# Optimization experiments

Measured on AMD Instinct MI355X. Metric: run time of the kernel, lower is better.

## Reference

```python
import jax, jax.numpy as jnp
import numpy as np

BITS = 256      # bits per token
HEADS = 8       # num voting heads
NPOS = 4        # n_position_bits for RELATIVE encoder (binary code of distance)
MAXD = 8        # max_distance of position encoder
NBPN = 12       # n_bits_per_neuron = min(similarity_bits, 12)
SEQ = 2048      # number of tokens
SIM = 2 * BITS + NPOS  # similarity_bits


def setup_inputs() -> dict:
    key = jax.random.key(0)
    k1, k2, k3 = jax.random.split(key, 3)
    tokens = jax.random.randint(k1, (SEQ, BITS), 0, 2, dtype=jnp.int32)
    head_idx = jax.random.randint(k2, (HEADS, NBPN), 0, SIM, dtype=jnp.int32)
    # RAM table contents: one bit (0/1) per address per head (trained lookup table)
    table = jax.random.bernoulli(k3, 0.5, (HEADS, 2 ** NBPN)).astype(jnp.float32)
    return {"tokens": tokens, "head_idx": head_idx, "table": table}


def reference(tokens, head_idx, table):
    S, B = tokens.shape
    H, K = head_idx.shape
    w = (2 ** jnp.arange(K)).astype(jnp.int32)  # slot weight 2^k per selected bit

    # relative-distance binary code table for distances 0..MAXD  -> (MAXD+1, NPOS)
    d_vals = jnp.arange(MAXD + 1)
    rel_bits = ((d_vals[:, None] >> jnp.arange(NPOS)[None, :]) & 1).astype(jnp.int32)

    # which source each selected bit position comes from within cat([query,key,rel])
    mask_q = (head_idx < B)
    mask_k = (head_idx >= B) & (head_idx < 2 * B)
    mask_r = head_idx >= 2 * B

    qg = tokens[:, jnp.clip(head_idx, 0, B - 1)]            # (S, H, K)
    kg = tokens[:, jnp.clip(head_idx - B, 0, B - 1)]        # (S, H, K)
    rg = rel_bits[:, jnp.clip(head_idx - 2 * B, 0, NPOS - 1)]  # (MAXD+1, H, K)

    # separable address contributions (query / key / relative distance)
    Aq = jnp.einsum('shk,hk->sh', qg, (mask_q * w).astype(jnp.int32))  # (S, H)
    Ak = jnp.einsum('shk,hk->sh', kg, (mask_k * w).astype(jnp.int32))  # (S, H)
    Ar = jnp.einsum('dhk,hk->dh', rg, (mask_r * w).astype(jnp.int32))  # (MAXD+1, H)

    i = jnp.arange(S)
    dist = jnp.clip(i[:, None] - i[None, :], 0, MAXD)        # (S, S)
    addr = Aq[:, None, :] + Ak[None, :, :] + Ar[dist]        # (S, S, H)

    head_votes = table[jnp.arange(H)[None, None, :], addr]   # (S, S, H)
    tril = (i[None, :] <= i[:, None]).astype(table.dtype)    # j > i gets vote 0
    votes = head_votes.sum(-1) * tril                        # (S, S)

    thr = H // 2
    attended = (votes >= thr).astype(table.dtype)            # (S, S)
    included = attended.sum(-1)                              # (S,)

    tok_f = tokens.astype(table.dtype)
    # XOR of selected tokens == per-bit parity of their sum
    parity = jnp.mod(attended @ tok_f, 2.0)                  # (S, B)
    # fallback: first token with max vote when nothing crossed the threshold
    fallback = tok_f[jnp.argmax(votes, axis=-1)]             # (S, B)
    return jnp.where((included > 0)[:, None], parity, fallback)
```

## Files before the change

kernel.cpp:

```cpp
#include <hip/hip_runtime.h>
#include <stdint.h>

#define SEQ   2048
#define BITS  256
#define HEADS 8
#define NPOS  4
#define MAXD  8
#define NBPN  12

typedef unsigned long long u64;
typedef unsigned int       u32;
typedef unsigned short     u16;

#define OFF_TBL    0
#define OFF_PACKED 4096
#define OFF_AQ     (4096 + 65536)
#define OFF_AK     (4096 + 65536 + 32768)
#define OFF_AR     (4096 + 65536 + 65536)

__global__ __launch_bounds__(256) void prep_kernel(
        const int* __restrict__ tokens, const int* __restrict__ head_idx,
        const float* __restrict__ table,
        u64* __restrict__ tblbits, u64* __restrict__ packed,
        u16* __restrict__ Aq, u16* __restrict__ Ak, u16* __restrict__ Ar) {
    const int bid = blockIdx.x, tid = threadIdx.x;
    if (bid < 2048) {
        int t = bid * 256 + tid;
        u64 m = __ballot(tokens[t] & 1);
        if ((tid & 63) == 0) packed[t >> 6] = m;
    } else if (bid < 2048 + 128) {
        int t = (bid - 2048) * 256 + tid;
        u64 m = __ballot(table[t] != 0.0f);
        if ((tid & 63) == 0) tblbits[t >> 6] = m;
    } else {
        int t = (bid - 2176) * 256 + tid;
        int s = t >> 3, h = t & 7;
        const int* hi  = head_idx + h * NBPN;
        const int* tok = tokens + s * BITS;
        int aq = 0, ak = 0;
        #pragma unroll
        for (int k = 0; k < NBPN; ++k) {
            int idx = hi[k];
            if (idx < BITS)          aq += tok[idx] << k;
            else if (idx < 2 * BITS) ak += tok[idx - BITS] << k;
        }
        Aq[t] = (u16)aq;
        Ak[t] = (u16)ak;
        if (t < (MAXD + 1) * HEADS) {
            int d = t / HEADS, hh = t % HEADS;
            const int* hi2 = head_idx + hh * NBPN;
            int ar = 0;
            #pragma unroll
            for (int k = 0; k < NBPN; ++k) {
                int idx = hi2[k];
                if (idx >= 2 * BITS) ar += ((d >> (idx - 2 * BITS)) & 1) << k;
            }
            Ar[t] = (u16)ar;
        }
    }
}

__device__ inline u64 shfl_down_u64(u64 x, int o) {
    u32 lo = (u32)x, hi = (u32)(x >> 32);
    lo = __shfl_down(lo, o, 64);
    hi = __shfl_down(hi, o, 64);
    return ((u64)hi << 32) | lo;
}

__global__ __launch_bounds__(128) void row_kernel(
        const u64* __restrict__ tblbits, const u64* __restrict__ packed,
        const u16* __restrict__ Aq, const u16* __restrict__ Ak,
        const u16* __restrict__ Ar, float* __restrict__ out) {

    __shared__ u32 tbl[HEADS * 128];
    __shared__ u16 aqar[MAXD + 1][HEADS];
    __shared__ u64 p_acc[2][4];
    __shared__ int p_inc[2];
    __shared__ u64 p_key[2];

    const int i   = blockIdx.x;
    const int tid = threadIdx.x;

    const u32* tb32 = (const u32*)tblbits;
    #pragma unroll
    for (int w = 0; w < 8; ++w) tbl[tid + w * 128] = tb32[tid + w * 128];
    if (tid < (MAXD + 1) * HEADS) {
        int h = tid & 7;
        aqar[tid >> 3][h] = (u16)(Aq[i * HEADS + h] + Ar[tid]);
    }
    __syncthreads();

    u32 a8[8];
    #pragma unroll
    for (int h = 0; h < 8; ++h) a8[h] = aqar[MAXD][h];

    u64 acc0 = 0, acc1 = 0, acc2 = 0, acc3 = 0;
    int inc = 0;
    u64 bestkey = 0;

    for (int j = tid; j <= i; j += 128) {
        int dist = i - j;
        const uint4 akv = *(const uint4*)(Ak + j * HEADS);
        int votes = 0;
        if (__any(dist < MAXD)) {
            #pragma unroll
            for (int h = 0; h < 8; ++h) {
                u32 ak_h = ((&akv.x)[h >> 1] >> ((h & 1) * 16)) & 0xFFFFu;
                u32 base = (dist >= MAXD) ? a8[h] : (u32)aqar[dist][h];
                u32 addr = base + ak_h;
                votes += (int)((tbl[(h << 7) + (addr >> 5)] >> (addr & 31)) & 1u);
            }
        } else {
            #pragma unroll
            for (int h = 0; h < 8; ++h) {
                u32 ak_h = ((&akv.x)[h >> 1] >> ((h & 1) * 16)) & 0xFFFFu;
                u32 addr = a8[h] + ak_h;
                votes += (int)((tbl[(h << 7) + (addr >> 5)] >> (addr & 31)) & 1u);
            }
        }
        int att = (votes >= HEADS / 2) ? 1 : 0;
        u64 m = (u64)0 - (u64)att;
        const ulonglong2* pj = (const ulonglong2*)(packed + j * 4);
        ulonglong2 pA = pj[0], pB = pj[1];
        acc0 ^= pA.x & m; acc1 ^= pA.y & m;
        acc2 ^= pB.x & m; acc3 ^= pB.y & m;
        inc += att;
        u64 key = ((u64)(votes + 1) << 32) | (u64)(0x7FFFFFFF - j);
        if (key > bestkey) bestkey = key;
    }

    #pragma unroll
    for (int o = 32; o > 0; o >>= 1) {
        acc0 ^= shfl_down_u64(acc0, o);
        acc1 ^= shfl_down_u64(acc1, o);
        acc2 ^= shfl_down_u64(acc2, o);
        acc3 ^= shfl_down_u64(acc3, o);
        inc  += __shfl_down(inc, o, 64);
        u64 k2 = shfl_down_u64(bestkey, o);
        if (k2 > bestkey) bestkey = k2;
    }
    int wave = tid >> 6;
    if ((tid & 63) == 0) {
        p_acc[wave][0] = acc0; p_acc[wave][1] = acc1;
        p_acc[wave][2] = acc2; p_acc[wave][3] = acc3;
        p_inc[wave] = inc; p_key[wave] = bestkey;
    }
    __syncthreads();

    u64 f0 = p_acc[0][0] ^ p_acc[1][0];
    u64 f1 = p_acc[0][1] ^ p_acc[1][1];
    u64 f2 = p_acc[0][2] ^ p_acc[1][2];
    u64 f3 = p_acc[0][3] ^ p_acc[1][3];
    int finc = p_inc[0] + p_inc[1];
    u64 fk = (p_key[0] > p_key[1]) ? p_key[0] : p_key[1];

    int b0  = tid * 2;
    int wsel = tid >> 5;
    u64 word;
    if (finc > 0) {
        word = (wsel < 2) ? (wsel == 0 ? f0 : f1) : (wsel == 2 ? f2 : f3);
    } else {
        int bestj = 0x7FFFFFFF - (int)(fk & 0xFFFFFFFFu);
        word = packed[bestj * 4 + wsel];
    }
    int sh = b0 & 63;
    float2 o2 = make_float2((float)((word >> sh) & 1ull),
                            (float)((word >> (sh + 1)) & 1ull));
    *(float2*)(out + i * BITS + b0) = o2;
}

extern "C" void kernel_launch(void* const* d_in, const int* in_sizes, int n_in,
                              void* d_out, int out_size, void* d_ws, size_t ws_size,
                              hipStream_t stream) {
    const int*   tokens   = (const int*)d_in[0];
    const int*   head_idx = (const int*)d_in[1];
    const float* table    = (const float*)d_in[2];
    float*       out      = (float*)d_out;
    char*        ws       = (char*)d_ws;

    u64* tblbits = (u64*)(ws + OFF_TBL);
    u64* packed  = (u64*)(ws + OFF_PACKED);
    u16* Aq      = (u16*)(ws + OFF_AQ);
    u16* Ak      = (u16*)(ws + OFF_AK);
    u16* Ar      = (u16*)(ws + OFF_AR);

    prep_kernel<<<2240, 256, 0, stream>>>(tokens, head_idx, table,
                                          tblbits, packed, Aq, Ak, Ar);
    row_kernel <<<SEQ, 128, 0, stream>>>(tblbits, packed, Aq, Ak, Ar, out);
}
```

Before: 76.43 us.

## Fuse prep and row kernels into one cooperative kernel with grid sync

Merges the bit-packing and address-precompute prep kernel into the row kernel and separates the two phases with a cooperative grid-wide sync. Aq and Ar now stay in shared memory instead of going through global memory, which saves a kernel launch and the related global traffic. The j loop is also unrolled by two with a predicated second iteration to raise instruction-level parallelism. In exchange, all 2048 blocks must be co-resident for the cooperative launch (launch_bounds 128,4), and the grid barrier adds its own cost.

```diff
diff --git a/kernel.cpp b/kernel.cpp
--- a/kernel.cpp
+++ b/kernel.cpp
@@ -1,5 +1,8 @@
 #include <hip/hip_runtime.h>
+#include <hip/hip_cooperative_groups.h>
 #include <stdint.h>
+
+namespace cg = cooperative_groups;
 
 #define SEQ   2048
 #define BITS  256
@@ -14,29 +17,47 @@
 
 #define OFF_TBL    0
 #define OFF_PACKED 4096
-#define OFF_AQ     (4096 + 65536)
-#define OFF_AK     (4096 + 65536 + 32768)
-#define OFF_AR     (4096 + 65536 + 65536)
-
-__global__ __launch_bounds__(256) void prep_kernel(
+#define OFF_AK     (4096 + 65536)
+
+__device__ inline u64 shfl_down_u64(u64 x, int o) {
+    u32 lo = (u32)x, hi = (u32)(x >> 32);
+    lo = __shfl_down(lo, o, 64);
+    hi = __shfl_down(hi, o, 64);
+    return ((u64)hi << 32) | lo;
+}
+
+__global__ __launch_bounds__(128, 4) void fused_kernel(
         const int* __restrict__ tokens, const int* __restrict__ head_idx,
         const float* __restrict__ table,
         u64* __restrict__ tblbits, u64* __restrict__ packed,
-        u16* __restrict__ Aq, u16* __restrict__ Ak, u16* __restrict__ Ar) {
-    const int bid = blockIdx.x, tid = threadIdx.x;
-    if (bid < 2048) {
-        int t = bid * 256 + tid;
-        u64 m = __ballot(tokens[t] & 1);
-        if ((tid & 63) == 0) packed[t >> 6] = m;
-    } else if (bid < 2048 + 128) {
-        int t = (bid - 2048) * 256 + tid;
-        u64 m = __ballot(table[t] != 0.0f);
-        if ((tid & 63) == 0) tblbits[t >> 6] = m;
-    } else {
-        int t = (bid - 2176) * 256 + tid;
-        int s = t >> 3, h = t & 7;
-        const int* hi  = head_idx + h * NBPN;
-        const int* tok = tokens + s * BITS;
+        u16* __restrict__ Ak, float* __restrict__ out) {
+
+    __shared__ u32 tbl[HEADS * 128];
+    __shared__ u16 aqar[MAXD + 1][HEADS];
+    __shared__ u16 s_aq[HEADS];
+    __shared__ u64 p_acc[2][4];
+    __shared__ int p_inc[2];
+    __shared__ u64 p_key[2];
+
+    const int b    = blockIdx.x;
+    const int tid  = threadIdx.x;
+    const int lane = tid & 63, wave = tid >> 6;
+
+    {
+        int c0 = b * 256 + wave * 64 + lane;
+        u64 m0 = __ballot(tokens[c0] & 1);
+        u64 m1 = __ballot(tokens[c0 + 128] & 1);
+        if (lane == 0) { packed[b * 4 + wave] = m0; packed[b * 4 + wave + 2] = m1; }
+    }
+    if (b < 128) {
+        int t0 = b * 256 + wave * 64 + lane;
+        u64 q0 = __ballot(table[t0] != 0.0f);
+        u64 q1 = __ballot(table[t0 + 128] != 0.0f);
+        if (lane == 0) { tblbits[b * 4 + wave] = q0; tblbits[b * 4 + wave + 2] = q1; }
+    }
+    if (tid < HEADS) {
+        const int* hi  = head_idx + tid * NBPN;
+        const int* tok = tokens + b * 256;
         int aq = 0, ak = 0;
         #pragma unroll
         for (int k = 0; k < NBPN; ++k) {
@@ -44,52 +65,31 @@
             if (idx < BITS)          aq += tok[idx] << k;
             else if (idx < 2 * BITS) ak += tok[idx - BITS] << k;
         }
-        Aq[t] = (u16)aq;
-        Ak[t] = (u16)ak;
-        if (t < (MAXD + 1) * HEADS) {
-            int d = t / HEADS, hh = t % HEADS;
-            const int* hi2 = head_idx + hh * NBPN;
-            int ar = 0;
-            #pragma unroll
-            for (int k = 0; k < NBPN; ++k) {
-                int idx = hi2[k];
-                if (idx >= 2 * BITS) ar += ((d >> (idx - 2 * BITS)) & 1) << k;
-            }
-            Ar[t] = (u16)ar;
-        }
-    }
-}
-
-__device__ inline u64 shfl_down_u64(u64 x, int o) {
-    u32 lo = (u32)x, hi = (u32)(x >> 32);
-    lo = __shfl_down(lo, o, 64);
-    hi = __shfl_down(hi, o, 64);
-    return ((u64)hi << 32) | lo;
-}
-
-__global__ __launch_bounds__(128) void row_kernel(
-        const u64* __restrict__ tblbits, const u64* __restrict__ packed,
-        const u16* __restrict__ Aq, const u16* __restrict__ Ak,
-        const u16* __restrict__ Ar, float* __restrict__ out) {
-
-    __shared__ u32 tbl[HEADS * 128];
-    __shared__ u16 aqar[MAXD + 1][HEADS];
-    __shared__ u64 p_acc[2][4];
-    __shared__ int p_inc[2];
-    __shared__ u64 p_key[2];
-
-    const int i   = blockIdx.x;
-    const int tid = threadIdx.x;
+        s_aq[tid] = (u16)aq;
+        Ak[b * HEADS + tid] = (u16)ak;
+    }
+    __syncthreads();
+    if (tid < (MAXD + 1) * HEADS) {
+        int d = tid >> 3, h = tid & 7;
+        const int* hi = head_idx + h * NBPN;
+        int ar = 0;
+        #pragma unroll
+        for (int k = 0; k < NBPN; ++k) {
+            int idx = hi[k];
+            if (idx >= 2 * BITS) ar += ((d >> (idx - 2 * BITS)) & 1) << k;
+        }
+        aqar[d][h] = (u16)(s_aq[h] + ar);
+    }
+
+    __threadfence();
+    cg::this_grid().sync();
 
     const u32* tb32 = (const u32*)tblbits;
     #pragma unroll
     for (int w = 0; w < 8; ++w) tbl[tid + w * 128] = tb32[tid + w * 128];
-    if (tid < (MAXD + 1) * HEADS) {
-        int h = tid & 7;
-        aqar[tid >> 3][h] = (u16)(Aq[i * HEADS + h] + Ar[tid]);
-    }
     __syncthreads();
 
+    const int i = b;
     u32 a8[8];
     #pragma unroll
     for (int h = 0; h < 8; ++h) a8[h] = aqar[MAXD][h];
@@ -98,35 +98,74 @@
     int inc = 0;
     u64 bestkey = 0;
 
-    for (int j = tid; j <= i; j += 128) {
-        int dist = i - j;
-        const uint4 akv = *(const uint4*)(Ak + j * HEADS);
-        int votes = 0;
-        if (__any(dist < MAXD)) {
-            #pragma unroll
-            for (int h = 0; h < 8; ++h) {
-                u32 ak_h = ((&akv.x)[h >> 1] >> ((h & 1) * 16)) & 0xFFFFu;
-                u32 base = (dist >= MAXD) ? a8[h] : (u32)aqar[dist][h];
-                u32 addr = base + ak_h;
-                votes += (int)((tbl[(h << 7) + (addr >> 5)] >> (addr & 31)) & 1u);
+    for (int j0 = tid; j0 <= i; j0 += 256) {
+        {
+            const int j = j0, dist = i - j;
+            const uint4 akv = *(const uint4*)(Ak + j * HEADS);
+            int votes = 0;
+            if (__any(dist < MAXD)) {
+                #pragma unroll
+                for (int h = 0; h < 8; ++h) {
+                    u32 ak_h = ((&akv.x)[h >> 1] >> ((h & 1) * 16)) & 0xFFFFu;
+                    u32 base = (dist >= MAXD) ? a8[h] : (u32)aqar[dist][h];
+                    u32 addr = base + ak_h;
+                    votes += (int)((tbl[(h << 7) + (addr >> 5)] >> (addr & 31)) & 1u);
+                }
+            } else {
+                #pragma unroll
+                for (int h = 0; h < 8; ++h) {
+                    u32 ak_h = ((&akv.x)[h >> 1] >> ((h & 1) * 16)) & 0xFFFFu;
+                    u32 addr = a8[h] + ak_h;
+                    votes += (int)((tbl[(h << 7) + (addr >> 5)] >> (addr & 31)) & 1u);
+                }
             }
-        } else {
-            #pragma unroll
-            for (int h = 0; h < 8; ++h) {
-                u32 ak_h = ((&akv.x)[h >> 1] >> ((h & 1) * 16)) & 0xFFFFu;
-                u32 addr = a8[h] + ak_h;
-                votes += (int)((tbl[(h << 7) + (addr >> 5)] >> (addr & 31)) & 1u);
+            int att = (votes >= HEADS / 2) ? 1 : 0;
+            u64 m = (u64)0 - (u64)att;
+            const ulonglong2* pj = (const ulonglong2*)(packed + j * 4);
+            ulonglong2 pA = pj[0], pB = pj[1];
+            acc0 ^= pA.x & m; acc1 ^= pA.y & m;
+            acc2 ^= pB.x & m; acc3 ^= pB.y & m;
+            inc += att;
+            u64 key = ((u64)(votes + 1) << 32) | (u64)(0x7FFFFFFF - j);
+            if (key > bestkey) bestkey = key;
+        }
+        {
+            const int jB = j0 + 128;
+            if (__any(jB <= i)) {
+                const bool v = (jB <= i);
+                const int j = v ? jB : i;
+                const int dist = i - j;
+                const uint4 akv = *(const uint4*)(Ak + j * HEADS);
+                int votes = 0;
+                if (__any(dist < MAXD)) {
+                    #pragma unroll
+                    for (int h = 0; h < 8; ++h) {
+                        u32 ak_h = ((&akv.x)[h >> 1] >> ((h & 1) * 16)) & 0xFFFFu;
+                        u32 base = (dist >= MAXD) ? a8[h] : (u32)aqar[dist][h];
+                        u32 addr = base + ak_h;
+                        votes += (int)((tbl[(h << 7) + (addr >> 5)] >> (addr & 31)) & 1u);
+                    }
+                } else {
+                    #pragma unroll
+                    for (int h = 0; h < 8; ++h) {
+                        u32 ak_h = ((&akv.x)[h >> 1] >> ((h & 1) * 16)) & 0xFFFFu;
+                        u32 addr = a8[h] + ak_h;
+                        votes += (int)((tbl[(h << 7) + (addr >> 5)] >> (addr & 31)) & 1u);
+                    }
+                }
+                int att = (v && votes >= HEADS / 2) ? 1 : 0;
+                u64 m = (u64)0 - (u64)att;
+                const ulonglong2* pj = (const ulonglong2*)(packed + j * 4);
+                ulonglong2 pA = pj[0], pB = pj[1];
+                acc0 ^= pA.x & m; acc1 ^= pA.y & m;
+                acc2 ^= pB.x & m; acc3 ^= pB.y & m;
+                inc += att;
+                if (v) {
+                    u64 key = ((u64)(votes + 1) << 32) | (u64)(0x7FFFFFFF - j);
+                    if (key > bestkey) bestkey = key;
+                }
             }
         }
-        int att = (votes >= HEADS / 2) ? 1 : 0;
-        u64 m = (u64)0 - (u64)att;
-        const ulonglong2* pj = (const ulonglong2*)(packed + j * 4);
-        ulonglong2 pA = pj[0], pB = pj[1];
-        acc0 ^= pA.x & m; acc1 ^= pA.y & m;
-        acc2 ^= pB.x & m; acc3 ^= pB.y & m;
-        inc += att;
-        u64 key = ((u64)(votes + 1) << 32) | (u64)(0x7FFFFFFF - j);
-        if (key > bestkey) bestkey = key;
     }
 
     #pragma unroll
@@ -139,8 +178,7 @@
         u64 k2 = shfl_down_u64(bestkey, o);
         if (k2 > bestkey) bestkey = k2;
     }
-    int wave = tid >> 6;
-    if ((tid & 63) == 0) {
+    if (lane == 0) {
         p_acc[wave][0] = acc0; p_acc[wave][1] = acc1;
         p_acc[wave][2] = acc2; p_acc[wave][3] = acc3;
         p_inc[wave] = inc; p_key[wave] = bestkey;
@@ -154,7 +192,7 @@
     int finc = p_inc[0] + p_inc[1];
     u64 fk = (p_key[0] > p_key[1]) ? p_key[0] : p_key[1];
 
-    int b0  = tid * 2;
+    int b0   = tid * 2;
     int wsel = tid >> 5;
     u64 word;
     if (finc > 0) {
@@ -180,11 +218,10 @@
 
     u64* tblbits = (u64*)(ws + OFF_TBL);
     u64* packed  = (u64*)(ws + OFF_PACKED);
-    u16* Aq      = (u16*)(ws + OFF_AQ);
     u16* Ak      = (u16*)(ws + OFF_AK);
-    u16* Ar      = (u16*)(ws + OFF_AR);
-
-    prep_kernel<<<2240, 256, 0, stream>>>(tokens, head_idx, table,
-                                          tblbits, packed, Aq, Ak, Ar);
-    row_kernel <<<SEQ, 128, 0, stream>>>(tblbits, packed, Aq, Ak, Ar, out);
+
+    void* args[] = { (void*)&tokens, (void*)&head_idx, (void*)&table,
+                     (void*)&tblbits, (void*)&packed, (void*)&Ak, (void*)&out };
+    hipLaunchCooperativeKernel((void*)fused_kernel, dim3(SEQ), dim3(128),
+                               args, 0, stream);
 }
```

Measured after the change: 258.4 us. +238.1%, slower.
